# Kernel tuning notes

Measured on AMD Instinct MI355X. Metric: run time of the kernel, lower is better.

Reference implementation:

```python
import jax, jax.numpy as jnp
import numpy as np

B, T, F, H = 2048, 512, 32, 128  # batch, seq_len, input_features, hidden_units

def _xavier(key, shape):
    fan_in, fan_out = shape[1], shape[0]
    limit = float(np.sqrt(6.0 / (fan_in + fan_out)))
    return jax.random.uniform(key, shape, jnp.float32, -limit, limit)

def setup_inputs() -> dict:
    key = jax.random.key(0)
    ks = jax.random.split(key, 8)
    x = jax.random.normal(ks[0], (B, T, F), jnp.float32)
    # PyTorch LSTM weights: weight_ih_l{k} [4H, in], weight_hh_l{k} [4H, H]; biases init to zeros.
    Wih0 = _xavier(ks[1], (4 * H, F))
    Whh0 = _xavier(ks[2], (4 * H, H))
    b0 = jnp.zeros((4 * H,), jnp.float32)  # b_ih + b_hh (both zero-init)
    Wih1 = _xavier(ks[3], (4 * H, H))
    Whh1 = _xavier(ks[4], (4 * H, H))
    b1 = jnp.zeros((4 * H,), jnp.float32)
    Wfc = _xavier(ks[5], (1, H))
    bfc = jnp.zeros((1,), jnp.float32)
    return dict(x=x, Wih0=Wih0, Whh0=Whh0, b0=b0, Wih1=Wih1, Whh1=Whh1, b1=b1, Wfc=Wfc, bfc=bfc)

def _lstm_layer(x, Wih, Whh, b):
    # x: [B, T, Din] -> outputs h over time: [B, T, H]
    pre = jnp.einsum('btf,gf->btg', x, Wih) + b  # precompute input projections [B, T, 4H]
    h0 = jnp.zeros((x.shape[0], Whh.shape[1]), x.dtype)

    def step(carry, p_t):
        h, c = carry
        z = p_t + h @ Whh.T  # [B, 4H]
        i, f, g, o = jnp.split(z, 4, axis=-1)  # PyTorch gate order: i, f, g, o
        i = jax.nn.sigmoid(i)
        f = jax.nn.sigmoid(f)
        g = jnp.tanh(g)
        o = jax.nn.sigmoid(o)
        c = f * c + i * g
        h = o * jnp.tanh(c)
        return (h, c), h

    (_, _), hs = jax.lax.scan(step, (h0, h0), jnp.swapaxes(pre, 0, 1))  # hs: [T, B, H]
    return jnp.swapaxes(hs, 0, 1)

def reference(x, Wih0, Whh0, b0, Wih1, Whh1, b1, Wfc, bfc):
    h = _lstm_layer(x, Wih0, Whh0, b0)   # layer 0 (dropout off in eval)
    h = _lstm_layer(h, Wih1, Whh1, b1)   # layer 1
    last = h[:, -1, :]                   # [B, H]
    return last @ Wfc.T + bfc            # [B, 1]
```

## Files before the change

kernel.cpp:

```cpp
#include <hip/hip_runtime.h>
#include <stdint.h>


#define B_ 2048
#define T_ 512
#define F_ 32
#define H_ 128
#define LSTR 144
#define H0SZ (8 * LSTR)
#define W1STR 8192

#define LOG2E 1.4426950408889634f

typedef _Float16 half8 __attribute__((ext_vector_type(8)));
typedef float float4_t __attribute__((ext_vector_type(4)));

#define BARRIER_LGKM() asm volatile("s_waitcnt lgkmcnt(0)\n\ts_barrier" ::: "memory")

__device__ __forceinline__ float fexp2(float x) {
  float r; asm("v_exp_f32 %0, %1" : "=v"(r) : "v"(x)); return r;
}
__device__ __forceinline__ float frcp(float x) { return __builtin_amdgcn_rcpf(x); }

__device__ __forceinline__ half8 cvt2f4(float4_t a, float4_t b) {
  half8 r;
  r[0] = (_Float16)a[0]; r[1] = (_Float16)a[1]; r[2] = (_Float16)a[2]; r[3] = (_Float16)a[3];
  r[4] = (_Float16)b[0]; r[5] = (_Float16)b[1]; r[6] = (_Float16)b[2]; r[7] = (_Float16)b[3];
  return r;
}
__device__ __forceinline__ half8 load8cvt(const float* p) {
  return cvt2f4(*(const float4_t*)p, *(const float4_t*)(p + 4));
}

__global__ __launch_bounds__(512, 2) void lstm_fused(
    const float* __restrict__ x, const float* __restrict__ Wih0,
    const float* __restrict__ Whh0, const float* __restrict__ b0,
    const float* __restrict__ Wih1, const float* __restrict__ Whh1,
    const float* __restrict__ b1, const float* __restrict__ Wfc,
    const float* __restrict__ bfc, float* __restrict__ out)
{
  __shared__ __attribute__((aligned(16))) _Float16 lds_w1[8 * W1STR];
  __shared__ __attribute__((aligned(16))) _Float16 lds_h0[2 * H0SZ];
  __shared__ __attribute__((aligned(16))) _Float16 lds_h1[2 * H0SZ];
  __shared__ float lds_fc[8][8];

  const int tid  = threadIdx.x;
  const int w    = tid >> 6;
  const int lane = tid & 63;
  const int n    = lane & 15;
  const int q    = lane >> 4;
  const int rbase = (int)blockIdx.x * 8;
  const int rload = rbase + (n & 7);
  const int rsh  = (q >> 1) * 2;
  const int rowq = (q & 1) * 4;
  const int colg = w * 16 + n;
  const int aoff = (n & 7) * LSTR + q * 8;

  half8 bwih0[4], bwhh0[4][4], bwhh1[4][4];
  _Float16* w1base = lds_w1 + w * W1STR + q * 128 + n * 8;
#pragma unroll
  for (int j = 0; j < 4; ++j) {
    const int g = j * H_ + colg;
    bwih0[j] = load8cvt(Wih0 + g * F_ + q * 8);
#pragma unroll
    for (int kc = 0; kc < 4; ++kc) {
      bwhh0[j][kc] = load8cvt(Whh0 + g * H_ + kc * 32 + q * 8);
      bwhh1[j][kc] = load8cvt(Whh1 + g * H_ + kc * 32 + q * 8);
      *(half8*)(w1base + (kc * 4 + j) * 512) = load8cvt(Wih1 + g * H_ + kc * 32 + q * 8);
    }
  }
  const float cI0 = -b0[0 * H_ + colg] * LOG2E;
  const float cF0 = -b0[1 * H_ + colg] * LOG2E;
  const float cG0 =  b0[2 * H_ + colg] * (2.0f * LOG2E);
  const float cO0 = -b0[3 * H_ + colg] * LOG2E;
  const float cI1 = -b1[0 * H_ + colg] * LOG2E;
  const float cF1 = -b1[1 * H_ + colg] * LOG2E;
  const float cG1 =  b1[2 * H_ + colg] * (2.0f * LOG2E);
  const float cO1 = -b1[3 * H_ + colg] * LOG2E;

  for (int i = tid; i < 2 * H0SZ; i += 512) { lds_h0[i] = (_Float16)0.0f; lds_h1[i] = (_Float16)0.0f; }
  __syncthreads();

  const float4_t zC = {0.f, 0.f, 0.f, 0.f};
  float c00 = 0.f, c01 = 0.f;
  float c10 = 0.f, c11 = 0.f;

  const float* xptr = x + rload * (T_ * F_) + q * 8;
  float4_t xrA = *(const float4_t*)(xptr);
  float4_t xrB = *(const float4_t*)(xptr + 4);

  auto GATES = [&](float4_t (&acc)[4], float cI, float cF, float cG, float cO,
                   float& ca, float& cb, _Float16* dst) {
#pragma unroll
    for (int rr = 0; rr < 2; ++rr) {
      const int ri = rsh + rr;
      const float gi = frcp(1.0f + fexp2(__builtin_fmaf(acc[0][ri], -LOG2E, cI)));
      const float gf = frcp(1.0f + fexp2(__builtin_fmaf(acc[1][ri], -LOG2E, cF)));
      const float gg = 1.0f - 2.0f * frcp(1.0f + fexp2(__builtin_fmaf(acc[2][ri], 2.0f * LOG2E, cG)));
      const float go = frcp(1.0f + fexp2(__builtin_fmaf(acc[3][ri], -LOG2E, cO)));
      float& cc = rr ? cb : ca;
      cc = __builtin_fmaf(gf, cc, gi * gg);
      const float th = 1.0f - 2.0f * frcp(1.0f + fexp2(cc * (2.0f * LOG2E)));
      dst[(rowq + ri) * LSTR + colg] = (_Float16)(go * th);
    }
  };

  {
    float4_t acc0[4];
    half8 ax = cvt2f4(xrA, xrB);
#pragma unroll
    for (int j = 0; j < 4; ++j)
      acc0[j] = __builtin_amdgcn_mfma_f32_16x16x32_f16(ax, bwih0[j], zC, 0, 0, 0);
    xrA = *(const float4_t*)(xptr + F_);
    xrB = *(const float4_t*)(xptr + F_ + 4);
    GATES(acc0, cI0, cF0, cG0, cO0, c00, c01, lds_h0 );
    BARRIER_LGKM();
  }

#pragma unroll 1
  for (int tau = 1; tau < T_; ++tau) {
    const int pw = tau & 1;
    _Float16* h0rd = lds_h0 + (pw ^ 1) * H0SZ;
    _Float16* h0wr = lds_h0 + pw * H0SZ;
    _Float16* h1rd = lds_h1 + pw * H0SZ;
    _Float16* h1wr = lds_h1 + (pw ^ 1) * H0SZ;

    half8 ah[4];
#pragma unroll
    for (int kc = 0; kc < 4; ++kc)
      ah[kc] = *(const half8*)(h0rd + aoff + kc * 32);
    half8 w1a[4];
#pragma unroll
    for (int j = 0; j < 4; ++j)
      w1a[j] = *(const half8*)(w1base + (0 * 4 + j) * 512);

    float4_t acc0[4];
    half8 ax = cvt2f4(xrA, xrB);
#pragma unroll
    for (int j = 0; j < 4; ++j)
      acc0[j] = __builtin_amdgcn_mfma_f32_16x16x32_f16(ax, bwih0[j], zC, 0, 0, 0);
#pragma unroll
    for (int kc = 0; kc < 4; ++kc)
#pragma unroll
      for (int j = 0; j < 4; ++j)
        acc0[j] = __builtin_amdgcn_mfma_f32_16x16x32_f16(ah[kc], bwhh0[j][kc], acc0[j], 0, 0, 0);
    const int tn = (tau + 1 < T_) ? tau + 1 : T_ - 1;
    xrA = *(const float4_t*)(xptr + tn * F_);
    xrB = *(const float4_t*)(xptr + tn * F_ + 4);

    float4_t acc1[4];
    half8 w1b[4];
#pragma unroll
    for (int j = 0; j < 4; ++j)
      w1b[j] = *(const half8*)(w1base + (1 * 4 + j) * 512);
#pragma unroll
    for (int j = 0; j < 4; ++j)
      acc1[j] = __builtin_amdgcn_mfma_f32_16x16x32_f16(ah[0], w1a[j], zC, 0, 0, 0);
#pragma unroll
    for (int j = 0; j < 4; ++j)
      w1a[j] = *(const half8*)(w1base + (2 * 4 + j) * 512);
#pragma unroll
    for (int j = 0; j < 4; ++j)
      acc1[j] = __builtin_amdgcn_mfma_f32_16x16x32_f16(ah[1], w1b[j], acc1[j], 0, 0, 0);
#pragma unroll
    for (int j = 0; j < 4; ++j)
      w1b[j] = *(const half8*)(w1base + (3 * 4 + j) * 512);
#pragma unroll
    for (int j = 0; j < 4; ++j)
      acc1[j] = __builtin_amdgcn_mfma_f32_16x16x32_f16(ah[2], w1a[j], acc1[j], 0, 0, 0);
#pragma unroll
    for (int j = 0; j < 4; ++j)
      acc1[j] = __builtin_amdgcn_mfma_f32_16x16x32_f16(ah[3], w1b[j], acc1[j], 0, 0, 0);

    GATES(acc0, cI0, cF0, cG0, cO0, c00, c01, h0wr);

    half8 a1h[4];
#pragma unroll
    for (int kc = 0; kc < 4; ++kc)
      a1h[kc] = *(const half8*)(h1rd + aoff + kc * 32);
#pragma unroll
    for (int kc = 0; kc < 4; ++kc)
#pragma unroll
      for (int j = 0; j < 4; ++j)
        acc1[j] = __builtin_amdgcn_mfma_f32_16x16x32_f16(a1h[kc], bwhh1[j][kc], acc1[j], 0, 0, 0);

    GATES(acc1, cI1, cF1, cG1, cO1, c10, c11, h1wr);
    BARRIER_LGKM();
  }

  {
    _Float16* h0rd = lds_h0 + H0SZ;
    _Float16* h1rd = lds_h1;
    _Float16* h1wr = lds_h1 + H0SZ;

    half8 ah[4];
#pragma unroll
    for (int kc = 0; kc < 4; ++kc)
      ah[kc] = *(const half8*)(h0rd + aoff + kc * 32);
    float4_t acc1[4];
    half8 w1a[4], w1b[4];
#pragma unroll
    for (int j = 0; j < 4; ++j)
      w1a[j] = *(const half8*)(w1base + (0 * 4 + j) * 512);
#pragma unroll
    for (int j = 0; j < 4; ++j)
      w1b[j] = *(const half8*)(w1base + (1 * 4 + j) * 512);
#pragma unroll
    for (int j = 0; j < 4; ++j)
      acc1[j] = __builtin_amdgcn_mfma_f32_16x16x32_f16(ah[0], w1a[j], zC, 0, 0, 0);
#pragma unroll
    for (int j = 0; j < 4; ++j)
      w1a[j] = *(const half8*)(w1base + (2 * 4 + j) * 512);
#pragma unroll
    for (int j = 0; j < 4; ++j)
      acc1[j] = __builtin_amdgcn_mfma_f32_16x16x32_f16(ah[1], w1b[j], acc1[j], 0, 0, 0);
#pragma unroll
    for (int j = 0; j < 4; ++j)
      w1b[j] = *(const half8*)(w1base + (3 * 4 + j) * 512);
#pragma unroll
    for (int j = 0; j < 4; ++j)
      acc1[j] = __builtin_amdgcn_mfma_f32_16x16x32_f16(ah[2], w1a[j], acc1[j], 0, 0, 0);
#pragma unroll
    for (int j = 0; j < 4; ++j)
      acc1[j] = __builtin_amdgcn_mfma_f32_16x16x32_f16(ah[3], w1b[j], acc1[j], 0, 0, 0);
    half8 a1h[4];
#pragma unroll
    for (int kc = 0; kc < 4; ++kc)
      a1h[kc] = *(const half8*)(h1rd + aoff + kc * 32);
#pragma unroll
    for (int kc = 0; kc < 4; ++kc)
#pragma unroll
      for (int j = 0; j < 4; ++j)
        acc1[j] = __builtin_amdgcn_mfma_f32_16x16x32_f16(a1h[kc], bwhh1[j][kc], acc1[j], 0, 0, 0);
    GATES(acc1, cI1, cF1, cG1, cO1, c10, c11, h1wr);
    asm volatile("s_waitcnt lgkmcnt(0)" ::: "memory");
  }

  const float wfcv = Wfc[colg];
  float p0 = (float)lds_h1[H0SZ + (rowq + rsh + 0) * LSTR + colg] * wfcv;
  float p1 = (float)lds_h1[H0SZ + (rowq + rsh + 1) * LSTR + colg] * wfcv;
#pragma unroll
  for (int m = 1; m < 16; m <<= 1) {
    p0 += __shfl_xor(p0, m);
    p1 += __shfl_xor(p1, m);
  }
  if (n == 0) {
    lds_fc[w][rowq + rsh + 0] = p0;
    lds_fc[w][rowq + rsh + 1] = p1;
  }
  __syncthreads();
  if (tid < 8) {
    float s = bfc[0];
#pragma unroll
    for (int wv = 0; wv < 8; ++wv) s += lds_fc[wv][tid];
    out[rbase + tid] = s;
  }
}

extern "C" void kernel_launch(void* const* d_in, const int* in_sizes, int n_in,
                              void* d_out, int out_size, void* d_ws, size_t ws_size,
                              hipStream_t stream) {
  const float* x    = (const float*)d_in[0];
  const float* Wih0 = (const float*)d_in[1];
  const float* Whh0 = (const float*)d_in[2];
  const float* b0   = (const float*)d_in[3];
  const float* Wih1 = (const float*)d_in[4];
  const float* Whh1 = (const float*)d_in[5];
  const float* b1   = (const float*)d_in[6];
  const float* Wfc  = (const float*)d_in[7];
  const float* bfc  = (const float*)d_in[8];
  float* outp = (float*)d_out;
  (void)d_ws; (void)ws_size;

  lstm_fused<<<B_ / 8, 512, 0, stream>>>(x, Wih0, Whh0, b0, Wih1, Whh1, b1,
                                         Wfc, bfc, outp);
}
```

Measured before the change: 998.1 us.

## Specialize waves per LSTM layer so layer 0 and layer 1 run pipelined

Splits the 8 waves of each block into two groups. Waves 0-3 compute only layer 0 and waves 4-7 compute only layer 1, each wave covering 32 hidden columns instead of 16. Layer 1 lags layer 0 by one timestep through the double-buffered LDS state, so the two layers are meant to overlap instead of running in sequence inside each wave. The cost is uneven work: layer-1 waves issue about 64 MFMAs per step against about 40 for layer-0 waves, and every wave still meets at one barrier per step, which may lengthen the critical path.

```diff
diff --git a/kernel.cpp b/kernel.cpp
--- a/kernel.cpp
+++ b/kernel.cpp
@@ -8,7 +8,8 @@
 #define H_ 128
 #define LSTR 144
 #define H0SZ (8 * LSTR)
-#define W1STR 8192
+#define W1SLOT 512
+#define W1WAVE (32 * W1SLOT)
 
 #define LOG2E 1.4426950408889634f
 
@@ -39,7 +40,7 @@
     const float* __restrict__ b1, const float* __restrict__ Wfc,
     const float* __restrict__ bfc, float* __restrict__ out)
 {
-  __shared__ __attribute__((aligned(16))) _Float16 lds_w1[8 * W1STR];
+  __shared__ __attribute__((aligned(16))) _Float16 lds_w1[4 * W1WAVE];
   __shared__ __attribute__((aligned(16))) _Float16 lds_h0[2 * H0SZ];
   __shared__ __attribute__((aligned(16))) _Float16 lds_h1[2 * H0SZ];
   __shared__ float lds_fc[8][8];
@@ -50,47 +51,20 @@
   const int n    = lane & 15;
   const int q    = lane >> 4;
   const int rbase = (int)blockIdx.x * 8;
-  const int rload = rbase + (n & 7);
   const int rsh  = (q >> 1) * 2;
   const int rowq = (q & 1) * 4;
-  const int colg = w * 16 + n;
+  const int wq   = w & 3;
+  const int hc0  = wq * 16 + n;
+  const int hc1  = hc0 + 64;
   const int aoff = (n & 7) * LSTR + q * 8;
-
-  half8 bwih0[4], bwhh0[4][4], bwhh1[4][4];
-  _Float16* w1base = lds_w1 + w * W1STR + q * 128 + n * 8;
-#pragma unroll
-  for (int j = 0; j < 4; ++j) {
-    const int g = j * H_ + colg;
-    bwih0[j] = load8cvt(Wih0 + g * F_ + q * 8);
-#pragma unroll
-    for (int kc = 0; kc < 4; ++kc) {
-      bwhh0[j][kc] = load8cvt(Whh0 + g * H_ + kc * 32 + q * 8);
-      bwhh1[j][kc] = load8cvt(Whh1 + g * H_ + kc * 32 + q * 8);
-      *(half8*)(w1base + (kc * 4 + j) * 512) = load8cvt(Wih1 + g * H_ + kc * 32 + q * 8);
-    }
-  }
-  const float cI0 = -b0[0 * H_ + colg] * LOG2E;
-  const float cF0 = -b0[1 * H_ + colg] * LOG2E;
-  const float cG0 =  b0[2 * H_ + colg] * (2.0f * LOG2E);
-  const float cO0 = -b0[3 * H_ + colg] * LOG2E;
-  const float cI1 = -b1[0 * H_ + colg] * LOG2E;
-  const float cF1 = -b1[1 * H_ + colg] * LOG2E;
-  const float cG1 =  b1[2 * H_ + colg] * (2.0f * LOG2E);
-  const float cO1 = -b1[3 * H_ + colg] * LOG2E;
-
-  for (int i = tid; i < 2 * H0SZ; i += 512) { lds_h0[i] = (_Float16)0.0f; lds_h1[i] = (_Float16)0.0f; }
-  __syncthreads();
+  const bool isL0 = (w < 4);
+
+  for (int i = tid; i < 2 * H0SZ; i += 512) lds_h1[i] = (_Float16)0.0f;
 
   const float4_t zC = {0.f, 0.f, 0.f, 0.f};
-  float c00 = 0.f, c01 = 0.f;
-  float c10 = 0.f, c11 = 0.f;
-
-  const float* xptr = x + rload * (T_ * F_) + q * 8;
-  float4_t xrA = *(const float4_t*)(xptr);
-  float4_t xrB = *(const float4_t*)(xptr + 4);
-
-  auto GATES = [&](float4_t (&acc)[4], float cI, float cF, float cG, float cO,
-                   float& ca, float& cb, _Float16* dst) {
+
+  auto GATES = [&](const float4_t (&acc)[4], float cI, float cF, float cG,
+                   float cO, float& ca, float& cb, _Float16* dst, int hcol) {
 #pragma unroll
     for (int rr = 0; rr < 2; ++rr) {
       const int ri = rsh + rr;
@@ -101,152 +75,227 @@
       float& cc = rr ? cb : ca;
       cc = __builtin_fmaf(gf, cc, gi * gg);
       const float th = 1.0f - 2.0f * frcp(1.0f + fexp2(cc * (2.0f * LOG2E)));
-      dst[(rowq + ri) * LSTR + colg] = (_Float16)(go * th);
+      dst[(rowq + ri) * LSTR + hcol] = (_Float16)(go * th);
     }
   };
 
-  {
-    float4_t acc0[4];
-    half8 ax = cvt2f4(xrA, xrB);
-#pragma unroll
-    for (int j = 0; j < 4; ++j)
-      acc0[j] = __builtin_amdgcn_mfma_f32_16x16x32_f16(ax, bwih0[j], zC, 0, 0, 0);
-    xrA = *(const float4_t*)(xptr + F_);
-    xrB = *(const float4_t*)(xptr + F_ + 4);
-    GATES(acc0, cI0, cF0, cG0, cO0, c00, c01, lds_h0 );
+  if (isL0) {
+    half8 bwih0[2][4], bwhh0[2][4][4];
+    float cI[2], cF[2], cG[2], cO[2];
+#pragma unroll
+    for (int grp = 0; grp < 2; ++grp) {
+      const int hcol = grp ? hc1 : hc0;
+#pragma unroll
+      for (int gt = 0; gt < 4; ++gt) {
+        const int g = gt * H_ + hcol;
+        bwih0[grp][gt] = load8cvt(Wih0 + g * F_ + q * 8);
+#pragma unroll
+        for (int kc = 0; kc < 4; ++kc)
+          bwhh0[grp][gt][kc] = load8cvt(Whh0 + g * H_ + kc * 32 + q * 8);
+      }
+      cI[grp] = -b0[0 * H_ + hcol] * LOG2E;
+      cF[grp] = -b0[1 * H_ + hcol] * LOG2E;
+      cG[grp] =  b0[2 * H_ + hcol] * (2.0f * LOG2E);
+      cO[grp] = -b0[3 * H_ + hcol] * LOG2E;
+    }
+    float c0a[2] = {0.f, 0.f}, c0b[2] = {0.f, 0.f};
+
+    const float* xptr = x + (rbase + (n & 7)) * (T_ * F_) + q * 8;
+    float4_t xrA = *(const float4_t*)(xptr);
+    float4_t xrB = *(const float4_t*)(xptr + 4);
+
+    {
+      half8 ax = cvt2f4(xrA, xrB);
+#pragma unroll
+      for (int grp = 0; grp < 2; ++grp) {
+        float4_t acc[4];
+#pragma unroll
+        for (int gt = 0; gt < 4; ++gt)
+          acc[gt] = __builtin_amdgcn_mfma_f32_16x16x32_f16(ax, bwih0[grp][gt], zC, 0, 0, 0);
+        GATES(acc, cI[grp], cF[grp], cG[grp], cO[grp], c0a[grp], c0b[grp],
+              lds_h0 , grp ? hc1 : hc0);
+      }
+      xrA = *(const float4_t*)(xptr + F_);
+      xrB = *(const float4_t*)(xptr + F_ + 4);
+      BARRIER_LGKM();
+    }
+
+#pragma unroll 1
+    for (int tau = 1; tau < T_; ++tau) {
+      const int pw = tau & 1;
+      _Float16* h0rd = lds_h0 + (pw ^ 1) * H0SZ;
+      _Float16* h0wr = lds_h0 + pw * H0SZ;
+
+      half8 ah[4];
+#pragma unroll
+      for (int kc = 0; kc < 4; ++kc)
+        ah[kc] = *(const half8*)(h0rd + aoff + kc * 32);
+      half8 ax = cvt2f4(xrA, xrB);
+
+#pragma unroll
+      for (int grp = 0; grp < 2; ++grp) {
+        float4_t acc[4];
+#pragma unroll
+        for (int gt = 0; gt < 4; ++gt)
+          acc[gt] = __builtin_amdgcn_mfma_f32_16x16x32_f16(ax, bwih0[grp][gt], zC, 0, 0, 0);
+#pragma unroll
+        for (int kc = 0; kc < 4; ++kc)
+#pragma unroll
+          for (int gt = 0; gt < 4; ++gt)
+            acc[gt] = __builtin_amdgcn_mfma_f32_16x16x32_f16(ah[kc], bwhh0[grp][gt][kc], acc[gt], 0, 0, 0);
+        if (grp == 0) {
+          const int tn = (tau + 1 < T_) ? tau + 1 : T_ - 1;
+          xrA = *(const float4_t*)(xptr + tn * F_);
+          xrB = *(const float4_t*)(xptr + tn * F_ + 4);
+        }
+        GATES(acc, cI[grp], cF[grp], cG[grp], cO[grp], c0a[grp], c0b[grp],
+              h0wr, grp ? hc1 : hc0);
+      }
+      BARRIER_LGKM();
+    }
+  } else {
+    half8 bwhh1[2][4][4];
+    float cI[2], cF[2], cG[2], cO[2];
+    _Float16* w1base = lds_w1 + wq * W1WAVE + q * 128 + n * 8;
+#pragma unroll
+    for (int grp = 0; grp < 2; ++grp) {
+      const int hcol = grp ? hc1 : hc0;
+#pragma unroll
+      for (int gt = 0; gt < 4; ++gt) {
+        const int g = gt * H_ + hcol;
+#pragma unroll
+        for (int kc = 0; kc < 4; ++kc) {
+          bwhh1[grp][gt][kc] = load8cvt(Whh1 + g * H_ + kc * 32 + q * 8);
+          *(half8*)(w1base + (grp * 16 + kc * 4 + gt) * W1SLOT) =
+              load8cvt(Wih1 + g * H_ + kc * 32 + q * 8);
+        }
+      }
+      cI[grp] = -b1[0 * H_ + hcol] * LOG2E;
+      cF[grp] = -b1[1 * H_ + hcol] * LOG2E;
+      cG[grp] =  b1[2 * H_ + hcol] * (2.0f * LOG2E);
+      cO[grp] = -b1[3 * H_ + hcol] * LOG2E;
+    }
+    float c1a[2] = {0.f, 0.f}, c1b[2] = {0.f, 0.f};
+
     BARRIER_LGKM();
+
+#pragma unroll 1
+    for (int tau = 1; tau < T_; ++tau) {
+      const int pw = tau & 1;
+      _Float16* h0rd = lds_h0 + (pw ^ 1) * H0SZ;
+      _Float16* h1rd = lds_h1 + pw * H0SZ;
+      _Float16* h1wr = lds_h1 + (pw ^ 1) * H0SZ;
+
+      half8 ah[4], a1h[4];
+#pragma unroll
+      for (int kc = 0; kc < 4; ++kc) {
+        ah[kc]  = *(const half8*)(h0rd + aoff + kc * 32);
+        a1h[kc] = *(const half8*)(h1rd + aoff + kc * 32);
+      }
+#pragma unroll
+      for (int grp = 0; grp < 2; ++grp) {
+        half8 wa[4], wb[4];
+        float4_t acc[4];
+#pragma unroll
+        for (int gt = 0; gt < 4; ++gt)
+          wa[gt] = *(const half8*)(w1base + (grp * 16 + 0 * 4 + gt) * W1SLOT);
+#pragma unroll
+        for (int gt = 0; gt < 4; ++gt)
+          wb[gt] = *(const half8*)(w1base + (grp * 16 + 1 * 4 + gt) * W1SLOT);
+#pragma unroll
+        for (int gt = 0; gt < 4; ++gt)
+          acc[gt] = __builtin_amdgcn_mfma_f32_16x16x32_f16(ah[0], wa[gt], zC, 0, 0, 0);
+#pragma unroll
+        for (int gt = 0; gt < 4; ++gt)
+          wa[gt] = *(const half8*)(w1base + (grp * 16 + 2 * 4 + gt) * W1SLOT);
+#pragma unroll
+        for (int gt = 0; gt < 4; ++gt)
+          acc[gt] = __builtin_amdgcn_mfma_f32_16x16x32_f16(ah[1], wb[gt], acc[gt], 0, 0, 0);
+#pragma unroll
+        for (int gt = 0; gt < 4; ++gt)
+          wb[gt] = *(const half8*)(w1base + (grp * 16 + 3 * 4 + gt) * W1SLOT);
+#pragma unroll
+        for (int gt = 0; gt < 4; ++gt)
+          acc[gt] = __builtin_amdgcn_mfma_f32_16x16x32_f16(ah[2], wa[gt], acc[gt], 0, 0, 0);
+#pragma unroll
+        for (int gt = 0; gt < 4; ++gt)
+          acc[gt] = __builtin_amdgcn_mfma_f32_16x16x32_f16(ah[3], wb[gt], acc[gt], 0, 0, 0);
+#pragma unroll
+        for (int kc = 0; kc < 4; ++kc)
+#pragma unroll
+          for (int gt = 0; gt < 4; ++gt)
+            acc[gt] = __builtin_amdgcn_mfma_f32_16x16x32_f16(a1h[kc], bwhh1[grp][gt][kc], acc[gt], 0, 0, 0);
+        GATES(acc, cI[grp], cF[grp], cG[grp], cO[grp], c1a[grp], c1b[grp],
+              h1wr, grp ? hc1 : hc0);
+      }
+      BARRIER_LGKM();
+    }
+
+    {
+      _Float16* h0rd = lds_h0 + H0SZ;
+      _Float16* h1rd = lds_h1;
+      _Float16* h1wr = lds_h1 + H0SZ;
+
+      half8 ah[4], a1h[4];
+#pragma unroll
+      for (int kc = 0; kc < 4; ++kc) {
+        ah[kc]  = *(const half8*)(h0rd + aoff + kc * 32);
+        a1h[kc] = *(const half8*)(h1rd + aoff + kc * 32);
+      }
+#pragma unroll
+      for (int grp = 0; grp < 2; ++grp) {
+        half8 wa[4], wb[4];
+        float4_t acc[4];
+#pragma unroll
+        for (int gt = 0; gt < 4; ++gt)
+          wa[gt] = *(const half8*)(w1base + (grp * 16 + 0 * 4 + gt) * W1SLOT);
+#pragma unroll
+        for (int gt = 0; gt < 4; ++gt)
+          wb[gt] = *(const half8*)(w1base + (grp * 16 + 1 * 4 + gt) * W1SLOT);
+#pragma unroll
+        for (int gt = 0; gt < 4; ++gt)
+          acc[gt] = __builtin_amdgcn_mfma_f32_16x16x32_f16(ah[0], wa[gt], zC, 0, 0, 0);
+#pragma unroll
+        for (int gt = 0; gt < 4; ++gt)
+          wa[gt] = *(const half8*)(w1base + (grp * 16 + 2 * 4 + gt) * W1SLOT);
+#pragma unroll
+        for (int gt = 0; gt < 4; ++gt)
+          acc[gt] = __builtin_amdgcn_mfma_f32_16x16x32_f16(ah[1], wb[gt], acc[gt], 0, 0, 0);
+#pragma unroll
+        for (int gt = 0; gt < 4; ++gt)
+          wb[gt] = *(const half8*)(w1base + (grp * 16 + 3 * 4 + gt) * W1SLOT);
+#pragma unroll
+        for (int gt = 0; gt < 4; ++gt)
+          acc[gt] = __builtin_amdgcn_mfma_f32_16x16x32_f16(ah[2], wa[gt], acc[gt], 0, 0, 0);
+#pragma unroll
+        for (int gt = 0; gt < 4; ++gt)
+          acc[gt] = __builtin_amdgcn_mfma_f32_16x16x32_f16(ah[3], wb[gt], acc[gt], 0, 0, 0);
+#pragma unroll
+        for (int kc = 0; kc < 4; ++kc)
+#pragma unroll
+          for (int gt = 0; gt < 4; ++gt)
+            acc[gt] = __builtin_amdgcn_mfma_f32_16x16x32_f16(a1h[kc], bwhh1[grp][gt][kc], acc[gt], 0, 0, 0);
+        GATES(acc, cI[grp], cF[grp], cG[grp], cO[grp], c1a[grp], c1b[grp],
+              h1wr, grp ? hc1 : hc0);
+      }
+      asm volatile("s_waitcnt lgkmcnt(0)" ::: "memory");
+    }
   }
 
-#pragma unroll 1
-  for (int tau = 1; tau < T_; ++tau) {
-    const int pw = tau & 1;
-    _Float16* h0rd = lds_h0 + (pw ^ 1) * H0SZ;
-    _Float16* h0wr = lds_h0 + pw * H0SZ;
-    _Float16* h1rd = lds_h1 + pw * H0SZ;
-    _Float16* h1wr = lds_h1 + (pw ^ 1) * H0SZ;
-
-    half8 ah[4];
-#pragma unroll
-    for (int kc = 0; kc < 4; ++kc)
-      ah[kc] = *(const half8*)(h0rd + aoff + kc * 32);
-    half8 w1a[4];
-#pragma unroll
-    for (int j = 0; j < 4; ++j)
-      w1a[j] = *(const half8*)(w1base + (0 * 4 + j) * 512);
-
-    float4_t acc0[4];
-    half8 ax = cvt2f4(xrA, xrB);
-#pragma unroll
-    for (int j = 0; j < 4; ++j)
-      acc0[j] = __builtin_amdgcn_mfma_f32_16x16x32_f16(ax, bwih0[j], zC, 0, 0, 0);
-#pragma unroll
-    for (int kc = 0; kc < 4; ++kc)
-#pragma unroll
-      for (int j = 0; j < 4; ++j)
-        acc0[j] = __builtin_amdgcn_mfma_f32_16x16x32_f16(ah[kc], bwhh0[j][kc], acc0[j], 0, 0, 0);
-    const int tn = (tau + 1 < T_) ? tau + 1 : T_ - 1;
-    xrA = *(const float4_t*)(xptr + tn * F_);
-    xrB = *(const float4_t*)(xptr + tn * F_ + 4);
-
-    float4_t acc1[4];
-    half8 w1b[4];
-#pragma unroll
-    for (int j = 0; j < 4; ++j)
-      w1b[j] = *(const half8*)(w1base + (1 * 4 + j) * 512);
-#pragma unroll
-    for (int j = 0; j < 4; ++j)
-      acc1[j] = __builtin_amdgcn_mfma_f32_16x16x32_f16(ah[0], w1a[j], zC, 0, 0, 0);
-#pragma unroll
-    for (int j = 0; j < 4; ++j)
-      w1a[j] = *(const half8*)(w1base + (2 * 4 + j) * 512);
-#pragma unroll
-    for (int j = 0; j < 4; ++j)
-      acc1[j] = __builtin_amdgcn_mfma_f32_16x16x32_f16(ah[1], w1b[j], acc1[j], 0, 0, 0);
-#pragma unroll
-    for (int j = 0; j < 4; ++j)
-      w1b[j] = *(const half8*)(w1base + (3 * 4 + j) * 512);
-#pragma unroll
-    for (int j = 0; j < 4; ++j)
-      acc1[j] = __builtin_amdgcn_mfma_f32_16x16x32_f16(ah[2], w1a[j], acc1[j], 0, 0, 0);
-#pragma unroll
-    for (int j = 0; j < 4; ++j)
-      acc1[j] = __builtin_amdgcn_mfma_f32_16x16x32_f16(ah[3], w1b[j], acc1[j], 0, 0, 0);
-
-    GATES(acc0, cI0, cF0, cG0, cO0, c00, c01, h0wr);
-
-    half8 a1h[4];
-#pragma unroll
-    for (int kc = 0; kc < 4; ++kc)
-      a1h[kc] = *(const half8*)(h1rd + aoff + kc * 32);
-#pragma unroll
-    for (int kc = 0; kc < 4; ++kc)
-#pragma unroll
-      for (int j = 0; j < 4; ++j)
-        acc1[j] = __builtin_amdgcn_mfma_f32_16x16x32_f16(a1h[kc], bwhh1[j][kc], acc1[j], 0, 0, 0);
-
-    GATES(acc1, cI1, cF1, cG1, cO1, c10, c11, h1wr);
-    BARRIER_LGKM();
-  }
-
-  {
-    _Float16* h0rd = lds_h0 + H0SZ;
-    _Float16* h1rd = lds_h1;
-    _Float16* h1wr = lds_h1 + H0SZ;
-
-    half8 ah[4];
-#pragma unroll
-    for (int kc = 0; kc < 4; ++kc)
-      ah[kc] = *(const half8*)(h0rd + aoff + kc * 32);
-    float4_t acc1[4];
-    half8 w1a[4], w1b[4];
-#pragma unroll
-    for (int j = 0; j < 4; ++j)
-      w1a[j] = *(const half8*)(w1base + (0 * 4 + j) * 512);
-#pragma unroll
-    for (int j = 0; j < 4; ++j)
-      w1b[j] = *(const half8*)(w1base + (1 * 4 + j) * 512);
-#pragma unroll
-    for (int j = 0; j < 4; ++j)
-      acc1[j] = __builtin_amdgcn_mfma_f32_16x16x32_f16(ah[0], w1a[j], zC, 0, 0, 0);
-#pragma unroll
-    for (int j = 0; j < 4; ++j)
-      w1a[j] = *(const half8*)(w1base + (2 * 4 + j) * 512);
-#pragma unroll
-    for (int j = 0; j < 4; ++j)
-      acc1[j] = __builtin_amdgcn_mfma_f32_16x16x32_f16(ah[1], w1b[j], acc1[j], 0, 0, 0);
-#pragma unroll
-    for (int j = 0; j < 4; ++j)
-      w1b[j] = *(const half8*)(w1base + (3 * 4 + j) * 512);
-#pragma unroll
-    for (int j = 0; j < 4; ++j)
-      acc1[j] = __builtin_amdgcn_mfma_f32_16x16x32_f16(ah[2], w1a[j], acc1[j], 0, 0, 0);
-#pragma unroll
-    for (int j = 0; j < 4; ++j)
-      acc1[j] = __builtin_amdgcn_mfma_f32_16x16x32_f16(ah[3], w1b[j], acc1[j], 0, 0, 0);
-    half8 a1h[4];
-#pragma unroll
-    for (int kc = 0; kc < 4; ++kc)
-      a1h[kc] = *(const half8*)(h1rd + aoff + kc * 32);
-#pragma unroll
-    for (int kc = 0; kc < 4; ++kc)
-#pragma unroll
-      for (int j = 0; j < 4; ++j)
-        acc1[j] = __builtin_amdgcn_mfma_f32_16x16x32_f16(a1h[kc], bwhh1[j][kc], acc1[j], 0, 0, 0);
-    GATES(acc1, cI1, cF1, cG1, cO1, c10, c11, h1wr);
-    asm volatile("s_waitcnt lgkmcnt(0)" ::: "memory");
-  }
-
+  __syncthreads();
+
+  const int colg = w * 16 + n;
   const float wfcv = Wfc[colg];
-  float p0 = (float)lds_h1[H0SZ + (rowq + rsh + 0) * LSTR + colg] * wfcv;
-  float p1 = (float)lds_h1[H0SZ + (rowq + rsh + 1) * LSTR + colg] * wfcv;
+  float p0 = (float)lds_h1[H0SZ + q * LSTR + colg] * wfcv;
+  float p1 = (float)lds_h1[H0SZ + (q + 4) * LSTR + colg] * wfcv;
 #pragma unroll
   for (int m = 1; m < 16; m <<= 1) {
     p0 += __shfl_xor(p0, m);
     p1 += __shfl_xor(p1, m);
   }
   if (n == 0) {
-    lds_fc[w][rowq + rsh + 0] = p0;
-    lds_fc[w][rowq + rsh + 1] = p1;
+    lds_fc[w][q] = p0;
+    lds_fc[w][q + 4] = p1;
   }
   __syncthreads();
   if (tid < 8) {
```

After: 968.4 us. 1.03x faster.

## Stream half of layer-1 input weights from global workspace instead of LDS

Applied to the files above, without the earlier changes.

When a workspace is available, half of the Wih1 fp16 fragments are written to global memory and reloaded every timestep into registers, overlapped with the layer-1 gate math. This halves the per-step LDS traffic for Wih1 and the LDS footprint, trading it for global/L2 reads each step. It also moves layer-0 gates earlier, ahead of the layer-1 MFMAs, and drops the initial zeroing of lds_h0. Every block writes the same weight image to the shared workspace, which is racy but benign because the values are identical; a block can read the image only after its own writes.

```diff
diff --git a/kernel.cpp b/kernel.cpp
--- a/kernel.cpp
+++ b/kernel.cpp
@@ -8,7 +8,6 @@
 #define H_ 128
 #define LSTR 144
 #define H0SZ (8 * LSTR)
-#define W1STR 8192
 
 #define LOG2E 1.4426950408889634f
 
@@ -32,14 +31,18 @@
   return cvt2f4(*(const float4_t*)p, *(const float4_t*)(p + 4));
 }
 
+template <bool WS>
 __global__ __launch_bounds__(512, 2) void lstm_fused(
     const float* __restrict__ x, const float* __restrict__ Wih0,
     const float* __restrict__ Whh0, const float* __restrict__ b0,
     const float* __restrict__ Wih1, const float* __restrict__ Whh1,
     const float* __restrict__ b1, const float* __restrict__ Wfc,
-    const float* __restrict__ bfc, float* __restrict__ out)
+    const float* __restrict__ bfc, _Float16* __restrict__ wimg,
+    float* __restrict__ out)
 {
-  __shared__ __attribute__((aligned(16))) _Float16 lds_w1[8 * W1STR];
+  constexpr int W1SLOTS = WS ? 8 : 16;
+  constexpr int W1WAVE  = W1SLOTS * 512;
+  __shared__ __attribute__((aligned(16))) _Float16 lds_w1[8 * W1WAVE + (WS ? 4096 : 0)];
   __shared__ __attribute__((aligned(16))) _Float16 lds_h0[2 * H0SZ];
   __shared__ __attribute__((aligned(16))) _Float16 lds_h1[2 * H0SZ];
   __shared__ float lds_fc[8][8];
@@ -50,14 +53,15 @@
   const int n    = lane & 15;
   const int q    = lane >> 4;
   const int rbase = (int)blockIdx.x * 8;
-  const int rload = rbase + (n & 7);
   const int rsh  = (q >> 1) * 2;
   const int rowq = (q & 1) * 4;
   const int colg = w * 16 + n;
   const int aoff = (n & 7) * LSTR + q * 8;
 
   half8 bwih0[4], bwhh0[4][4], bwhh1[4][4];
-  _Float16* w1base = lds_w1 + w * W1STR + q * 128 + n * 8;
+  _Float16* w1base = lds_w1 + w * W1WAVE + q * 128 + n * 8;
+  half8* wsw = (half8*)wimg + lane;
+  const half8* wsp = (const half8*)wimg + lane;
 #pragma unroll
   for (int j = 0; j < 4; ++j) {
     const int g = j * H_ + colg;
@@ -66,7 +70,16 @@
     for (int kc = 0; kc < 4; ++kc) {
       bwhh0[j][kc] = load8cvt(Whh0 + g * H_ + kc * 32 + q * 8);
       bwhh1[j][kc] = load8cvt(Whh1 + g * H_ + kc * 32 + q * 8);
-      *(half8*)(w1base + (kc * 4 + j) * 512) = load8cvt(Wih1 + g * H_ + kc * 32 + q * 8);
+    }
+    if constexpr (WS) {
+      wsw[(((w << 2) + j) * 2 + 0) * 64] = load8cvt(Wih1 + g * H_ + 0 * 32 + q * 8);
+      wsw[(((w << 2) + j) * 2 + 1) * 64] = load8cvt(Wih1 + g * H_ + 1 * 32 + q * 8);
+      *(half8*)(w1base + (0 * 4 + j) * 512) = load8cvt(Wih1 + g * H_ + 2 * 32 + q * 8);
+      *(half8*)(w1base + (1 * 4 + j) * 512) = load8cvt(Wih1 + g * H_ + 3 * 32 + q * 8);
+    } else {
+#pragma unroll
+      for (int kc = 0; kc < 4; ++kc)
+        *(half8*)(w1base + (kc * 4 + j) * 512) = load8cvt(Wih1 + g * H_ + kc * 32 + q * 8);
     }
   }
   const float cI0 = -b0[0 * H_ + colg] * LOG2E;
@@ -78,19 +91,19 @@
   const float cG1 =  b1[2 * H_ + colg] * (2.0f * LOG2E);
   const float cO1 = -b1[3 * H_ + colg] * LOG2E;
 
-  for (int i = tid; i < 2 * H0SZ; i += 512) { lds_h0[i] = (_Float16)0.0f; lds_h1[i] = (_Float16)0.0f; }
+  for (int i = tid; i < 2 * H0SZ; i += 512) lds_h1[i] = (_Float16)0.0f;
   __syncthreads();
 
   const float4_t zC = {0.f, 0.f, 0.f, 0.f};
   float c00 = 0.f, c01 = 0.f;
   float c10 = 0.f, c11 = 0.f;
 
-  const float* xptr = x + rload * (T_ * F_) + q * 8;
+  const float* xptr = x + (rbase + (n & 7)) * (T_ * F_) + q * 8;
   float4_t xrA = *(const float4_t*)(xptr);
   float4_t xrB = *(const float4_t*)(xptr + 4);
 
-  auto GATES = [&](float4_t (&acc)[4], float cI, float cF, float cG, float cO,
-                   float& ca, float& cb, _Float16* dst) {
+  auto GATES = [&](const float4_t (&acc)[4], float cI, float cF, float cG,
+                   float cO, float& ca, float& cb, _Float16* dst) {
 #pragma unroll
     for (int rr = 0; rr < 2; ++rr) {
       const int ri = rsh + rr;
@@ -105,6 +118,8 @@
     }
   };
 
+  half8 wA[4], wB[4];
+
   {
     float4_t acc0[4];
     half8 ax = cvt2f4(xrA, xrB);
@@ -114,6 +129,13 @@
     xrA = *(const float4_t*)(xptr + F_);
     xrB = *(const float4_t*)(xptr + F_ + 4);
     GATES(acc0, cI0, cF0, cG0, cO0, c00, c01, lds_h0 );
+    if constexpr (WS) {
+#pragma unroll
+      for (int j = 0; j < 4; ++j) {
+        wA[j] = wsp[(((w << 2) + j) * 2 + 0) * 64];
+        wB[j] = wsp[(((w << 2) + j) * 2 + 1) * 64];
+      }
+    }
     BARRIER_LGKM();
   }
 
@@ -129,13 +151,9 @@
 #pragma unroll
     for (int kc = 0; kc < 4; ++kc)
       ah[kc] = *(const half8*)(h0rd + aoff + kc * 32);
-    half8 w1a[4];
-#pragma unroll
-    for (int j = 0; j < 4; ++j)
-      w1a[j] = *(const half8*)(w1base + (0 * 4 + j) * 512);
+    half8 ax = cvt2f4(xrA, xrB);
 
     float4_t acc0[4];
-    half8 ax = cvt2f4(xrA, xrB);
 #pragma unroll
     for (int j = 0; j < 4; ++j)
       acc0[j] = __builtin_amdgcn_mfma_f32_16x16x32_f16(ax, bwih0[j], zC, 0, 0, 0);
@@ -147,43 +165,50 @@
     const int tn = (tau + 1 < T_) ? tau + 1 : T_ - 1;
     xrA = *(const float4_t*)(xptr + tn * F_);
     xrB = *(const float4_t*)(xptr + tn * F_ + 4);
+    GATES(acc0, cI0, cF0, cG0, cO0, c00, c01, h0wr);
 
     float4_t acc1[4];
-    half8 w1b[4];
-#pragma unroll
-    for (int j = 0; j < 4; ++j)
-      w1b[j] = *(const half8*)(w1base + (1 * 4 + j) * 512);
-#pragma unroll
-    for (int j = 0; j < 4; ++j)
-      acc1[j] = __builtin_amdgcn_mfma_f32_16x16x32_f16(ah[0], w1a[j], zC, 0, 0, 0);
-#pragma unroll
-    for (int j = 0; j < 4; ++j)
-      w1a[j] = *(const half8*)(w1base + (2 * 4 + j) * 512);
-#pragma unroll
-    for (int j = 0; j < 4; ++j)
-      acc1[j] = __builtin_amdgcn_mfma_f32_16x16x32_f16(ah[1], w1b[j], acc1[j], 0, 0, 0);
-#pragma unroll
-    for (int j = 0; j < 4; ++j)
-      w1b[j] = *(const half8*)(w1base + (3 * 4 + j) * 512);
-#pragma unroll
-    for (int j = 0; j < 4; ++j)
-      acc1[j] = __builtin_amdgcn_mfma_f32_16x16x32_f16(ah[2], w1a[j], acc1[j], 0, 0, 0);
-#pragma unroll
-    for (int j = 0; j < 4; ++j)
-      acc1[j] = __builtin_amdgcn_mfma_f32_16x16x32_f16(ah[3], w1b[j], acc1[j], 0, 0, 0);
-
-    GATES(acc0, cI0, cF0, cG0, cO0, c00, c01, h0wr);
-
+    if constexpr (!WS) {
+#pragma unroll
+      for (int j = 0; j < 4; ++j) wA[j] = *(const half8*)(w1base + (0 * 4 + j) * 512);
+#pragma unroll
+      for (int j = 0; j < 4; ++j) wB[j] = *(const half8*)(w1base + (1 * 4 + j) * 512);
+    }
+#pragma unroll
+    for (int j = 0; j < 4; ++j)
+      acc1[j] = __builtin_amdgcn_mfma_f32_16x16x32_f16(ah[0], wA[j], zC, 0, 0, 0);
+    half8 wC[4], wD[4];
+#pragma unroll
+    for (int j = 0; j < 4; ++j)
+      wC[j] = *(const half8*)(w1base + ((WS ? 0 : 2) * 4 + j) * 512);
+#pragma unroll
+    for (int j = 0; j < 4; ++j)
+      acc1[j] = __builtin_amdgcn_mfma_f32_16x16x32_f16(ah[1], wB[j], acc1[j], 0, 0, 0);
+#pragma unroll
+    for (int j = 0; j < 4; ++j)
+      wD[j] = *(const half8*)(w1base + ((WS ? 1 : 3) * 4 + j) * 512);
     half8 a1h[4];
 #pragma unroll
     for (int kc = 0; kc < 4; ++kc)
       a1h[kc] = *(const half8*)(h1rd + aoff + kc * 32);
+#pragma unroll
+    for (int j = 0; j < 4; ++j)
+      acc1[j] = __builtin_amdgcn_mfma_f32_16x16x32_f16(ah[2], wC[j], acc1[j], 0, 0, 0);
+#pragma unroll
+    for (int j = 0; j < 4; ++j)
+      acc1[j] = __builtin_amdgcn_mfma_f32_16x16x32_f16(ah[3], wD[j], acc1[j], 0, 0, 0);
 #pragma unroll
     for (int kc = 0; kc < 4; ++kc)
 #pragma unroll
       for (int j = 0; j < 4; ++j)
         acc1[j] = __builtin_amdgcn_mfma_f32_16x16x32_f16(a1h[kc], bwhh1[j][kc], acc1[j], 0, 0, 0);
-
+    if constexpr (WS) {
+#pragma unroll
+      for (int j = 0; j < 4; ++j) {
+        wA[j] = wsp[(((w << 2) + j) * 2 + 0) * 64];
+        wB[j] = wsp[(((w << 2) + j) * 2 + 1) * 64];
+      }
+    }
     GATES(acc1, cI1, cF1, cG1, cO1, c10, c11, h1wr);
     BARRIER_LGKM();
   }
@@ -193,40 +218,38 @@
     _Float16* h1rd = lds_h1;
     _Float16* h1wr = lds_h1 + H0SZ;
 
-    half8 ah[4];
-#pragma unroll
-    for (int kc = 0; kc < 4; ++kc)
-      ah[kc] = *(const half8*)(h0rd + aoff + kc * 32);
+    half8 ah[4], a1h[4];
+#pragma unroll
+    for (int kc = 0; kc < 4; ++kc) {
+      ah[kc]  = *(const half8*)(h0rd + aoff + kc * 32);
+      a1h[kc] = *(const half8*)(h1rd + aoff + kc * 32);
+    }
     float4_t acc1[4];
-    half8 w1a[4], w1b[4];
-#pragma unroll
-    for (int j = 0; j < 4; ++j)
-      w1a[j] = *(const half8*)(w1base + (0 * 4 + j) * 512);
-#pragma unroll
-    for (int j = 0; j < 4; ++j)
-      w1b[j] = *(const half8*)(w1base + (1 * 4 + j) * 512);
-#pragma unroll
-    for (int j = 0; j < 4; ++j)
-      acc1[j] = __builtin_amdgcn_mfma_f32_16x16x32_f16(ah[0], w1a[j], zC, 0, 0, 0);
-#pragma unroll
-    for (int j = 0; j < 4; ++j)
-      w1a[j] = *(const half8*)(w1base + (2 * 4 + j) * 512);
-#pragma unroll
-    for (int j = 0; j < 4; ++j)
-      acc1[j] = __builtin_amdgcn_mfma_f32_16x16x32_f16(ah[1], w1b[j], acc1[j], 0, 0, 0);
-#pragma unroll
-    for (int j = 0; j < 4; ++j)
-      w1b[j] = *(const half8*)(w1base + (3 * 4 + j) * 512);
-#pragma unroll
-    for (int j = 0; j < 4; ++j)
-      acc1[j] = __builtin_amdgcn_mfma_f32_16x16x32_f16(ah[2], w1a[j], acc1[j], 0, 0, 0);
-#pragma unroll
-    for (int j = 0; j < 4; ++j)
-      acc1[j] = __builtin_amdgcn_mfma_f32_16x16x32_f16(ah[3], w1b[j], acc1[j], 0, 0, 0);
-    half8 a1h[4];
-#pragma unroll
-    for (int kc = 0; kc < 4; ++kc)
-      a1h[kc] = *(const half8*)(h1rd + aoff + kc * 32);
+    if constexpr (!WS) {
+#pragma unroll
+      for (int j = 0; j < 4; ++j) wA[j] = *(const half8*)(w1base + (0 * 4 + j) * 512);
+#pragma unroll
+      for (int j = 0; j < 4; ++j) wB[j] = *(const half8*)(w1base + (1 * 4 + j) * 512);
+    }
+#pragma unroll
+    for (int j = 0; j < 4; ++j)
+      acc1[j] = __builtin_amdgcn_mfma_f32_16x16x32_f16(ah[0], wA[j], zC, 0, 0, 0);
+    half8 wC[4], wD[4];
+#pragma unroll
+    for (int j = 0; j < 4; ++j)
+      wC[j] = *(const half8*)(w1base + ((WS ? 0 : 2) * 4 + j) * 512);
+#pragma unroll
+    for (int j = 0; j < 4; ++j)
+      acc1[j] = __builtin_amdgcn_mfma_f32_16x16x32_f16(ah[1], wB[j], acc1[j], 0, 0, 0);
+#pragma unroll
+    for (int j = 0; j < 4; ++j)
+      wD[j] = *(const half8*)(w1base + ((WS ? 1 : 3) * 4 + j) * 512);
+#pragma unroll
+    for (int j = 0; j < 4; ++j)
+      acc1[j] = __builtin_amdgcn_mfma_f32_16x16x32_f16(ah[2], wC[j], acc1[j], 0, 0, 0);
+#pragma unroll
+    for (int j = 0; j < 4; ++j)
+      acc1[j] = __builtin_amdgcn_mfma_f32_16x16x32_f16(ah[3], wD[j], acc1[j], 0, 0, 0);
 #pragma unroll
     for (int kc = 0; kc < 4; ++kc)
 #pragma unroll
@@ -235,6 +258,7 @@
     GATES(acc1, cI1, cF1, cG1, cO1, c10, c11, h1wr);
     asm volatile("s_waitcnt lgkmcnt(0)" ::: "memory");
   }
+  __syncthreads();
 
   const float wfcv = Wfc[colg];
   float p0 = (float)lds_h1[H0SZ + (rowq + rsh + 0) * LSTR + colg] * wfcv;
@@ -270,8 +294,15 @@
   const float* Wfc  = (const float*)d_in[7];
   const float* bfc  = (const float*)d_in[8];
   float* outp = (float*)d_out;
-  (void)d_ws; (void)ws_size;
-
-  lstm_fused<<<B_ / 8, 512, 0, stream>>>(x, Wih0, Whh0, b0, Wih1, Whh1, b1,
-                                         Wfc, bfc, outp);
-}
+  (void)in_sizes; (void)n_in; (void)out_size;
+
+  if (d_ws != nullptr && ws_size >= 65536) {
+    lstm_fused<true><<<B_ / 8, 512, 0, stream>>>(x, Wih0, Whh0, b0, Wih1, Whh1,
+                                                 b1, Wfc, bfc, (_Float16*)d_ws,
+                                                 outp);
+  } else {
+    lstm_fused<false><<<B_ / 8, 512, 0, stream>>>(x, Wih0, Whh0, b0, Wih1, Whh1,
+                                                  b1, Wfc, bfc, (_Float16*)nullptr,
+                                                  outp);
+  }
+}
```

Result: slower. 1.128 ms (+13.0%).

## Alternate layer-0/layer-1 section order between even and odd waves to stagger MFMA and transcendental work

Applied to the files above, without the earlier changes.

Splits each timestep into a layer-0 section and a layer-1 section. Even waves run layer 0 first and odd waves run layer 1 first, so waves sharing a SIMD are out of phase: one issues MFMAs while another evaluates the exp/rcp gate math. This aims to keep the matrix and vector ALUs busy together instead of every wave hitting the same phase at once. It adds a wave-uniform branch, changes the interleaving of the Wih1 LDS loads, and adds a __syncthreads before the final FC reduction.

```diff
diff --git a/kernel.cpp b/kernel.cpp
--- a/kernel.cpp
+++ b/kernel.cpp
@@ -50,11 +50,11 @@
   const int n    = lane & 15;
   const int q    = lane >> 4;
   const int rbase = (int)blockIdx.x * 8;
-  const int rload = rbase + (n & 7);
   const int rsh  = (q >> 1) * 2;
   const int rowq = (q & 1) * 4;
   const int colg = w * 16 + n;
   const int aoff = (n & 7) * LSTR + q * 8;
+  const bool wEven = (__builtin_amdgcn_readfirstlane(w & 1) == 0);
 
   half8 bwih0[4], bwhh0[4][4], bwhh1[4][4];
   _Float16* w1base = lds_w1 + w * W1STR + q * 128 + n * 8;
@@ -85,12 +85,12 @@
   float c00 = 0.f, c01 = 0.f;
   float c10 = 0.f, c11 = 0.f;
 
-  const float* xptr = x + rload * (T_ * F_) + q * 8;
+  const float* xptr = x + (rbase + (n & 7)) * (T_ * F_) + q * 8;
   float4_t xrA = *(const float4_t*)(xptr);
   float4_t xrB = *(const float4_t*)(xptr + 4);
 
-  auto GATES = [&](float4_t (&acc)[4], float cI, float cF, float cG, float cO,
-                   float& ca, float& cb, _Float16* dst) {
+  auto GATES = [&](const float4_t (&acc)[4], float cI, float cF, float cG,
+                   float cO, float& ca, float& cb, _Float16* dst) {
 #pragma unroll
     for (int rr = 0; rr < 2; ++rr) {
       const int ri = rsh + rr;
@@ -105,6 +105,62 @@
     }
   };
 
+  auto L0SEC = [&](const half8 (&ah)[4], _Float16* h0wr, int tau) {
+    float4_t acc0[4];
+    half8 ax = cvt2f4(xrA, xrB);
+#pragma unroll
+    for (int j = 0; j < 4; ++j)
+      acc0[j] = __builtin_amdgcn_mfma_f32_16x16x32_f16(ax, bwih0[j], zC, 0, 0, 0);
+#pragma unroll
+    for (int kc = 0; kc < 4; ++kc)
+#pragma unroll
+      for (int j = 0; j < 4; ++j)
+        acc0[j] = __builtin_amdgcn_mfma_f32_16x16x32_f16(ah[kc], bwhh0[j][kc], acc0[j], 0, 0, 0);
+    const int tn = (tau + 1 < T_) ? tau + 1 : T_ - 1;
+    xrA = *(const float4_t*)(xptr + tn * F_);
+    xrB = *(const float4_t*)(xptr + tn * F_ + 4);
+    GATES(acc0, cI0, cF0, cG0, cO0, c00, c01, h0wr);
+  };
+
+  auto L1SEC = [&](const half8 (&ah)[4], _Float16* h1rd, _Float16* h1wr) {
+    float4_t acc1[4];
+    half8 w1a[4], w1b[4];
+#pragma unroll
+    for (int j = 0; j < 4; ++j)
+      w1a[j] = *(const half8*)(w1base + (0 * 4 + j) * 512);
+#pragma unroll
+    for (int j = 0; j < 4; ++j)
+      w1b[j] = *(const half8*)(w1base + (1 * 4 + j) * 512);
+#pragma unroll
+    for (int j = 0; j < 4; ++j)
+      acc1[j] = __builtin_amdgcn_mfma_f32_16x16x32_f16(ah[0], w1a[j], zC, 0, 0, 0);
+#pragma unroll
+    for (int j = 0; j < 4; ++j)
+      w1a[j] = *(const half8*)(w1base + (2 * 4 + j) * 512);
+#pragma unroll
+    for (int j = 0; j < 4; ++j)
+      acc1[j] = __builtin_amdgcn_mfma_f32_16x16x32_f16(ah[1], w1b[j], acc1[j], 0, 0, 0);
+#pragma unroll
+    for (int j = 0; j < 4; ++j)
+      w1b[j] = *(const half8*)(w1base + (3 * 4 + j) * 512);
+#pragma unroll
+    for (int j = 0; j < 4; ++j)
+      acc1[j] = __builtin_amdgcn_mfma_f32_16x16x32_f16(ah[2], w1a[j], acc1[j], 0, 0, 0);
+    half8 a1h[4];
+#pragma unroll
+    for (int kc = 0; kc < 4; ++kc)
+      a1h[kc] = *(const half8*)(h1rd + aoff + kc * 32);
+#pragma unroll
+    for (int j = 0; j < 4; ++j)
+      acc1[j] = __builtin_amdgcn_mfma_f32_16x16x32_f16(ah[3], w1b[j], acc1[j], 0, 0, 0);
+#pragma unroll
+    for (int kc = 0; kc < 4; ++kc)
+#pragma unroll
+      for (int j = 0; j < 4; ++j)
+        acc1[j] = __builtin_amdgcn_mfma_f32_16x16x32_f16(a1h[kc], bwhh1[j][kc], acc1[j], 0, 0, 0);
+    GATES(acc1, cI1, cF1, cG1, cO1, c10, c11, h1wr);
+  };
+
   {
     float4_t acc0[4];
     half8 ax = cvt2f4(xrA, xrB);
@@ -129,62 +185,14 @@
 #pragma unroll
     for (int kc = 0; kc < 4; ++kc)
       ah[kc] = *(const half8*)(h0rd + aoff + kc * 32);
-    half8 w1a[4];
-#pragma unroll
-    for (int j = 0; j < 4; ++j)
-      w1a[j] = *(const half8*)(w1base + (0 * 4 + j) * 512);
-
-    float4_t acc0[4];
-    half8 ax = cvt2f4(xrA, xrB);
-#pragma unroll
-    for (int j = 0; j < 4; ++j)
-      acc0[j] = __builtin_amdgcn_mfma_f32_16x16x32_f16(ax, bwih0[j], zC, 0, 0, 0);
-#pragma unroll
-    for (int kc = 0; kc < 4; ++kc)
-#pragma unroll
-      for (int j = 0; j < 4; ++j)
-        acc0[j] = __builtin_amdgcn_mfma_f32_16x16x32_f16(ah[kc], bwhh0[j][kc], acc0[j], 0, 0, 0);
-    const int tn = (tau + 1 < T_) ? tau + 1 : T_ - 1;
-    xrA = *(const float4_t*)(xptr + tn * F_);
-    xrB = *(const float4_t*)(xptr + tn * F_ + 4);
-
-    float4_t acc1[4];
-    half8 w1b[4];
-#pragma unroll
-    for (int j = 0; j < 4; ++j)
-      w1b[j] = *(const half8*)(w1base + (1 * 4 + j) * 512);
-#pragma unroll
-    for (int j = 0; j < 4; ++j)
-      acc1[j] = __builtin_amdgcn_mfma_f32_16x16x32_f16(ah[0], w1a[j], zC, 0, 0, 0);
-#pragma unroll
-    for (int j = 0; j < 4; ++j)
-      w1a[j] = *(const half8*)(w1base + (2 * 4 + j) * 512);
-#pragma unroll
-    for (int j = 0; j < 4; ++j)
-      acc1[j] = __builtin_amdgcn_mfma_f32_16x16x32_f16(ah[1], w1b[j], acc1[j], 0, 0, 0);
-#pragma unroll
-    for (int j = 0; j < 4; ++j)
-      w1b[j] = *(const half8*)(w1base + (3 * 4 + j) * 512);
-#pragma unroll
-    for (int j = 0; j < 4; ++j)
-      acc1[j] = __builtin_amdgcn_mfma_f32_16x16x32_f16(ah[2], w1a[j], acc1[j], 0, 0, 0);
-#pragma unroll
-    for (int j = 0; j < 4; ++j)
-      acc1[j] = __builtin_amdgcn_mfma_f32_16x16x32_f16(ah[3], w1b[j], acc1[j], 0, 0, 0);
-
-    GATES(acc0, cI0, cF0, cG0, cO0, c00, c01, h0wr);
-
-    half8 a1h[4];
-#pragma unroll
-    for (int kc = 0; kc < 4; ++kc)
-      a1h[kc] = *(const half8*)(h1rd + aoff + kc * 32);
-#pragma unroll
-    for (int kc = 0; kc < 4; ++kc)
-#pragma unroll
-      for (int j = 0; j < 4; ++j)
-        acc1[j] = __builtin_amdgcn_mfma_f32_16x16x32_f16(a1h[kc], bwhh1[j][kc], acc1[j], 0, 0, 0);
-
-    GATES(acc1, cI1, cF1, cG1, cO1, c10, c11, h1wr);
+
+    if (wEven) {
+      L0SEC(ah, h0wr, tau);
+      L1SEC(ah, h1rd, h1wr);
+    } else {
+      L1SEC(ah, h1rd, h1wr);
+      L0SEC(ah, h0wr, tau);
+    }
     BARRIER_LGKM();
   }
 
@@ -192,49 +200,14 @@
     _Float16* h0rd = lds_h0 + H0SZ;
     _Float16* h1rd = lds_h1;
     _Float16* h1wr = lds_h1 + H0SZ;
-
     half8 ah[4];
 #pragma unroll
     for (int kc = 0; kc < 4; ++kc)
       ah[kc] = *(const half8*)(h0rd + aoff + kc * 32);
-    float4_t acc1[4];
-    half8 w1a[4], w1b[4];
-#pragma unroll
-    for (int j = 0; j < 4; ++j)
-      w1a[j] = *(const half8*)(w1base + (0 * 4 + j) * 512);
-#pragma unroll
-    for (int j = 0; j < 4; ++j)
-      w1b[j] = *(const half8*)(w1base + (1 * 4 + j) * 512);
-#pragma unroll
-    for (int j = 0; j < 4; ++j)
-      acc1[j] = __builtin_amdgcn_mfma_f32_16x16x32_f16(ah[0], w1a[j], zC, 0, 0, 0);
-#pragma unroll
-    for (int j = 0; j < 4; ++j)
-      w1a[j] = *(const half8*)(w1base + (2 * 4 + j) * 512);
-#pragma unroll
-    for (int j = 0; j < 4; ++j)
-      acc1[j] = __builtin_amdgcn_mfma_f32_16x16x32_f16(ah[1], w1b[j], acc1[j], 0, 0, 0);
-#pragma unroll
-    for (int j = 0; j < 4; ++j)
-      w1b[j] = *(const half8*)(w1base + (3 * 4 + j) * 512);
-#pragma unroll
-    for (int j = 0; j < 4; ++j)
-      acc1[j] = __builtin_amdgcn_mfma_f32_16x16x32_f16(ah[2], w1a[j], acc1[j], 0, 0, 0);
-#pragma unroll
-    for (int j = 0; j < 4; ++j)
-      acc1[j] = __builtin_amdgcn_mfma_f32_16x16x32_f16(ah[3], w1b[j], acc1[j], 0, 0, 0);
-    half8 a1h[4];
-#pragma unroll
-    for (int kc = 0; kc < 4; ++kc)
-      a1h[kc] = *(const half8*)(h1rd + aoff + kc * 32);
-#pragma unroll
-    for (int kc = 0; kc < 4; ++kc)
-#pragma unroll
-      for (int j = 0; j < 4; ++j)
-        acc1[j] = __builtin_amdgcn_mfma_f32_16x16x32_f16(a1h[kc], bwhh1[j][kc], acc1[j], 0, 0, 0);
-    GATES(acc1, cI1, cF1, cG1, cO1, c10, c11, h1wr);
+    L1SEC(ah, h1rd, h1wr);
     asm volatile("s_waitcnt lgkmcnt(0)" ::: "memory");
   }
+  __syncthreads();
 
   const float wfcv = Wfc[colg];
   float p0 = (float)lds_h1[H0SZ + (rowq + rsh + 0) * LSTR + colg] * wfcv;
```

After: 1.024 ms. 2.5% more time.
